# Performance work log

Hardware: AMD Instinct MI355X
Metric: run time of the kernel (lower is better)

## Reference

```python
import jax, jax.numpy as jnp
import numpy as np

HIDDEN = 1024
HEADS = 16
HEAD_DIM = HIDDEN // HEADS


def setup_inputs() -> dict:
    key = jax.random.key(0)
    ks = jax.random.split(key, 9)
    s = 1.0 / np.sqrt(HIDDEN)
    inp = {
        "x": jax.random.normal(ks[0], (4, 2048, HIDDEN), dtype=jnp.float32),
        "wq": jax.random.uniform(ks[1], (HIDDEN, HIDDEN), jnp.float32, -s, s),
        "bq": jax.random.uniform(ks[2], (HIDDEN,), jnp.float32, -s, s),
        "wk": jax.random.uniform(ks[3], (HIDDEN, HIDDEN), jnp.float32, -s, s),
        "bk": jax.random.uniform(ks[4], (HIDDEN,), jnp.float32, -s, s),
        "wv": jax.random.uniform(ks[5], (HIDDEN, HIDDEN), jnp.float32, -s, s),
        "bv": jax.random.uniform(ks[6], (HIDDEN,), jnp.float32, -s, s),
        "wo": jax.random.uniform(ks[7], (HIDDEN, HIDDEN), jnp.float32, -s, s),
        "bo": jax.random.uniform(ks[8], (HIDDEN,), jnp.float32, -s, s),
    }
    return inp


def reference(x, wq, bq, wk, bk, wv, bv, wo, bo):
    B, S, D = x.shape
    H, Hd = HEADS, HEAD_DIM
    # torch Linear: y = x @ W.T + b
    def split_heads(t):  # [B,S,D] -> [B,H,S,Hd]
        return t.reshape(B, S, H, Hd).transpose(0, 2, 1, 3)
    q = split_heads(x @ wq.T + bq)
    k = split_heads(x @ wk.T + bk)
    v = split_heads(x @ wv.T + bv)
    scores = jnp.einsum('bhqd,bhkd->bhqk', q, k) / jnp.sqrt(jnp.float32(Hd))
    attn = jax.nn.softmax(scores, axis=-1)  # dropout is identity in eval
    ctx = jnp.einsum('bhqk,bhkd->bhqd', attn, v)
    ctx = ctx.transpose(0, 2, 1, 3).reshape(B, S, D)
    pooled = ctx.mean(axis=1)  # [B, D]
    out = pooled @ wo.T + bo
    return out, attn.mean(axis=1)
```

## Files before the change

### kernel.cpp

```cpp
#include <hip/hip_runtime.h>

#define B_ 4
#define S_ 2048
#define D_ 1024
#define H_ 16
#define HD_ 64
#define M_ 8192

typedef __attribute__((ext_vector_type(8))) short          bf16x8;
typedef __attribute__((ext_vector_type(8))) unsigned short u16x8;
typedef __attribute__((ext_vector_type(4))) float          f32x4;

#define MFMA16(a, b, c) __builtin_amdgcn_mfma_f32_16x16x32_bf16((a), (b), (c), 0, 0, 0)

#define SCL 0.18033688011112042f

__device__ __forceinline__ unsigned short f2b(float f) {
    unsigned int u = __float_as_uint(f);
    return (unsigned short)((u + 0x7fffu + ((u >> 16) & 1u)) >> 16);
}

__device__ __forceinline__ unsigned int cvtpk_bf16(float lo, float hi) {
    unsigned int r;
    asm("v_cvt_pk_bf16_f32 %0, %1, %2" : "=v"(r) : "v"(lo), "v"(hi));
    return r;
}

__global__ __launch_bounds__(256) void cast_k(const float* __restrict__ src,
                                              unsigned short* __restrict__ dst, int n) {
    int i = (blockIdx.x * 256 + threadIdx.x) * 4;
    if (i >= n) return;
    float4 v = *(const float4*)(src + i);
    ushort4 o;
    o.x = f2b(v.x); o.y = f2b(v.y); o.z = f2b(v.z); o.w = f2b(v.w);
    *(ushort4*)(dst + i) = o;
}

__global__ __launch_bounds__(256) void cast3_k(
    const float* __restrict__ s0, const float* __restrict__ s1, const float* __restrict__ s2,
    unsigned short* __restrict__ d0, unsigned short* __restrict__ d1,
    unsigned short* __restrict__ d2, int n) {
    const float* src = (blockIdx.y == 0) ? s0 : (blockIdx.y == 1) ? s1 : s2;
    unsigned short* dst = (blockIdx.y == 0) ? d0 : (blockIdx.y == 1) ? d1 : d2;
    int i = (blockIdx.x * 256 + threadIdx.x) * 4;
    if (i >= n) return;
    float4 v = *(const float4*)(src + i);
    ushort4 o;
    o.x = f2b(v.x); o.y = f2b(v.y); o.z = f2b(v.z); o.w = f2b(v.w);
    *(ushort4*)(dst + i) = o;
}

__global__ __launch_bounds__(256) void qkv_gemm_k(
    const unsigned short* __restrict__ xb,
    const unsigned short* __restrict__ wb0, const unsigned short* __restrict__ wb1,
    const unsigned short* __restrict__ wb2,
    const float* __restrict__ bq, const float* __restrict__ bk, const float* __restrict__ bv,
    unsigned short* __restrict__ Qo, unsigned short* __restrict__ Ko,
    unsigned short* __restrict__ VT)
{
    __shared__ unsigned short xs[128][72];
    __shared__ unsigned short wsm[128][72];

    const unsigned short* W; const float* bias;
    if (blockIdx.z == 0)      { W = wb0; bias = bq; }
    else if (blockIdx.z == 1) { W = wb1; bias = bk; }
    else                      { W = wb2; bias = bv; }

    const int m0 = blockIdx.x * 128, n0 = blockIdx.y * 128;
    const int tid = threadIdx.x, lane = tid & 63, wid = tid >> 6;
    const int wm = (wid >> 1) * 64, wn = (wid & 1) * 64;
    const int srow = tid >> 3;
    const int skc  = (tid & 7) * 8;

    f32x4 acc[4][4] = {};

    for (int k0 = 0; k0 < D_; k0 += 64) {
        u16x8 xa[4], wa[4];
        #pragma unroll
        for (int r = 0; r < 4; ++r) {
            int row = srow + 32 * r;
            xa[r] = *(const u16x8*)&xb[(size_t)(m0 + row) * D_ + k0 + skc];
            wa[r] = *(const u16x8*)&W [(size_t)(n0 + row) * D_ + k0 + skc];
        }
        __syncthreads();
        #pragma unroll
        for (int r = 0; r < 4; ++r) {
            int row = srow + 32 * r;
            *(u16x8*)&xs[row][skc]  = xa[r];
            *(u16x8*)&wsm[row][skc] = wa[r];
        }
        __syncthreads();
        #pragma unroll
        for (int kd = 0; kd < 2; ++kd) {
            const int kc = 32 * kd + 8 * (lane >> 4);
            bf16x8 af[4], bfr[4];
            #pragma unroll
            for (int mf = 0; mf < 4; ++mf)
                af[mf] = *(const bf16x8*)&xs[wm + 16 * mf + (lane & 15)][kc];
            #pragma unroll
            for (int nf = 0; nf < 4; ++nf)
                bfr[nf] = *(const bf16x8*)&wsm[wn + 16 * nf + (lane & 15)][kc];
            #pragma unroll
            for (int mf = 0; mf < 4; ++mf)
                #pragma unroll
                for (int nf = 0; nf < 4; ++nf)
                    acc[mf][nf] = MFMA16(af[mf], bfr[nf], acc[mf][nf]);
        }
    }

    const int col_l = lane & 15, rgrp = lane >> 4;
    if (blockIdx.z != 2) {
        unsigned short* out = (blockIdx.z == 0) ? Qo : Ko;
        const float oscale = (blockIdx.z == 0) ? SCL : 1.0f;
        #pragma unroll
        for (int nf = 0; nf < 4; ++nf) {
            const int n = n0 + wn + 16 * nf + col_l;
            const float bval = bias[n];
            const int h = n >> 6, d = n & 63;
            #pragma unroll
            for (int mf = 0; mf < 4; ++mf)
                #pragma unroll
                for (int r = 0; r < 4; ++r) {
                    int m = m0 + wm + 16 * mf + 4 * rgrp + r;
                    int bI = m >> 11, s = m & 2047;
                    out[(((size_t)bI * H_ + h) * S_ + s) * HD_ + d]
                        = f2b((acc[mf][nf][r] + bval) * oscale);
                }
        }
    } else {
        #pragma unroll
        for (int nf = 0; nf < 4; ++nf) {
            const int n = n0 + wn + 16 * nf + col_l;
            const float bval = bias[n];
            const int h = n >> 6, d = n & 63;
            #pragma unroll
            for (int mf = 0; mf < 4; ++mf) {
                int m = m0 + wm + 16 * mf + 4 * rgrp;
                int bI = m >> 11, s = m & 2047;
                ushort4 o;
                o.x = f2b(acc[mf][nf][0] + bval);
                o.y = f2b(acc[mf][nf][1] + bval);
                o.z = f2b(acc[mf][nf][2] + bval);
                o.w = f2b(acc[mf][nf][3] + bval);
                *(ushort4*)&VT[(((size_t)bI * H_ + h) * HD_ + d) * S_ + s] = o;
            }
        }
    }
}

__global__ __launch_bounds__(256) void attn_ctx_k(
    const unsigned short* __restrict__ Q, const unsigned short* __restrict__ K,
    const unsigned short* __restrict__ VT,
    float* __restrict__ L, float* __restrict__ PPOOL)
{
    __shared__ unsigned short ks[64][72];
    __shared__ unsigned short vt[64][72];
    __shared__ unsigned short ps[128][72];
    __shared__ float pp[4][64];
    __shared__ float lsm[4][32];

    const int lin = blockIdx.x;
    const int g   = (lin & 7) | ((lin >> 7) << 3);
    const int qb  = (lin >> 3) & 15;
    const int b   = g >> 4, h = g & 15;
    const int q0  = qb * 128;

    const size_t hoff = ((size_t)(b * H_ + h)) * S_ * HD_;
    const unsigned short* Qh  = Q  + hoff;
    const unsigned short* Kh  = K  + hoff;
    const unsigned short* VTh = VT + hoff;

    const int tid = threadIdx.x, lane = tid & 63, wid = tid >> 6;
    const int srow = tid >> 3;
    const int skc  = (tid & 7) * 8;
    const int col_l = lane & 15, rgrp = lane >> 4;

    bf16x8 qf[2][2];
    #pragma unroll
    for (int i = 0; i < 2; ++i)
        #pragma unroll
        for (int kd = 0; kd < 2; ++kd)
            qf[i][kd] = *(const bf16x8*)&Qh[(size_t)(q0 + 32 * wid + 16 * i + col_l) * HD_
                                            + 32 * kd + 8 * rgrp];

    f32x4 cacc[2][4] = {};
    float lp[2] = {};

    for (int kb = 0; kb < S_; kb += 64) {
        u16x8 ka[2], va[2];
        #pragma unroll
        for (int r = 0; r < 2; ++r) {
            int row = srow + 32 * r;
            ka[r] = *(const u16x8*)&Kh [(size_t)(kb + row) * HD_ + skc];
            va[r] = *(const u16x8*)&VTh[(size_t)row * S_ + kb + skc];
        }
        __syncthreads();
        #pragma unroll
        for (int r = 0; r < 2; ++r) {
            int row = srow + 32 * r;
            *(u16x8*)&ks[row][skc] = ka[r];
            *(u16x8*)&vt[row][skc] = va[r];
        }
        __syncthreads();

        #pragma unroll
        for (int n = 0; n < 4; ++n) {
            f32x4 s0 = {}, s1 = {};
            #pragma unroll
            for (int kd = 0; kd < 2; ++kd) {
                const int kc = 32 * kd + 8 * rgrp;
                bf16x8 kf = *(const bf16x8*)&ks[16 * n + col_l][kc];
                s0 = MFMA16(kf, qf[0][kd], s0);
                s1 = MFMA16(kf, qf[1][kd], s1);
            }
            float e0 = exp2f(s0[0]), e1 = exp2f(s0[1]), e2 = exp2f(s0[2]), e3 = exp2f(s0[3]);
            lp[0] += (e0 + e1) + (e2 + e3);
            uint2 w0 = { cvtpk_bf16(e0, e1), cvtpk_bf16(e2, e3) };
            *(uint2*)&ps[32 * wid + col_l][16 * n + 4 * rgrp] = w0;
            float f0 = exp2f(s1[0]), f1 = exp2f(s1[1]), f2 = exp2f(s1[2]), f3 = exp2f(s1[3]);
            lp[1] += (f0 + f1) + (f2 + f3);
            uint2 w1 = { cvtpk_bf16(f0, f1), cvtpk_bf16(f2, f3) };
            *(uint2*)&ps[32 * wid + 16 + col_l][16 * n + 4 * rgrp] = w1;
        }

        #pragma unroll
        for (int kk = 0; kk < 2; ++kk) {
            const int kc = 32 * kk + 8 * rgrp;
            bf16x8 pa[2], vf[4];
            #pragma unroll
            for (int i = 0; i < 2; ++i)
                pa[i] = *(const bf16x8*)&ps[32 * wid + 16 * i + col_l][kc];
            #pragma unroll
            for (int n = 0; n < 4; ++n)
                vf[n] = *(const bf16x8*)&vt[16 * n + col_l][kc];
            #pragma unroll
            for (int i = 0; i < 2; ++i)
                #pragma unroll
                for (int n = 0; n < 4; ++n)
                    cacc[i][n] = MFMA16(pa[i], vf[n], cacc[i][n]);
        }
    }

    #pragma unroll
    for (int i = 0; i < 2; ++i) {
        float v = lp[i];
        v += __shfl_xor(v, 16); v += __shfl_xor(v, 32);
        lp[i] = v;
    }
    if (lane < 16) {
        #pragma unroll
        for (int i = 0; i < 2; ++i) {
            L[((size_t)(b * H_ + h)) * S_ + q0 + 32 * wid + 16 * i + lane] = lp[i];
            lsm[wid][16 * i + lane] = lp[i];
        }
    }

    float pool4[4] = {};
    #pragma unroll
    for (int i = 0; i < 2; ++i)
        #pragma unroll
        for (int r = 0; r < 4; ++r) {
            float inv = 1.0f / lsm[wid][16 * i + 4 * rgrp + r];
            #pragma unroll
            for (int n = 0; n < 4; ++n)
                pool4[n] = fmaf(cacc[i][n][r], inv, pool4[n]);
        }
    #pragma unroll
    for (int n = 0; n < 4; ++n) {
        float v = pool4[n];
        v += __shfl_xor(v, 16); v += __shfl_xor(v, 32);
        pool4[n] = v;
    }
    if (lane < 16) {
        #pragma unroll
        for (int n = 0; n < 4; ++n) pp[wid][16 * n + lane] = pool4[n];
    }
    __syncthreads();
    if (tid < 64) {
        float s = pp[0][tid] + pp[1][tid] + pp[2][tid] + pp[3][tid];
        PPOOL[((size_t)(b * H_ + h) * (S_ / 128) + qb) * 64 + tid] = s;
    }
}

__global__ __launch_bounds__(256) void attn_mean_k(
    const unsigned short* __restrict__ Q, const unsigned short* __restrict__ K,
    const float* __restrict__ L, float* __restrict__ attn_out)
{
    __shared__ unsigned short qs[128][72];
    __shared__ unsigned short ksm[64][72];
    __shared__ float lsm[128];

    const int k0 = blockIdx.x * 64, q0 = blockIdx.y * 128, b = blockIdx.z;
    const int tid = threadIdx.x, lane = tid & 63, wid = tid >> 6;
    const int col_l = lane & 15, rgrp = lane >> 4;
    const int qrow = tid >> 1, qcol = (tid & 1) * 32;
    const int krow = tid >> 2, kcol = (tid & 3) * 16;

    f32x4 macc[4][2] = {};

    for (int h = 0; h < H_; ++h) {
        const size_t hoff = ((size_t)(b * H_ + h)) * S_ * HD_;
        const unsigned short* Qh = Q + hoff;
        const unsigned short* Kh = K + hoff;

        u16x8 qa[4], ka[2];
        #pragma unroll
        for (int j = 0; j < 4; ++j)
            qa[j] = *(const u16x8*)&Qh[(size_t)(q0 + qrow) * HD_ + qcol + 8 * j];
        #pragma unroll
        for (int j = 0; j < 2; ++j)
            ka[j] = *(const u16x8*)&Kh[(size_t)(k0 + krow) * HD_ + kcol + 8 * j];
        float lval = 0.f;
        if (tid < 128) lval = L[((size_t)(b * H_ + h)) * S_ + q0 + tid];

        __syncthreads();
        #pragma unroll
        for (int j = 0; j < 4; ++j) *(u16x8*)&qs[qrow][qcol + 8 * j] = qa[j];
        #pragma unroll
        for (int j = 0; j < 2; ++j) *(u16x8*)&ksm[krow][kcol + 8 * j] = ka[j];
        if (tid < 128) lsm[tid] = lval;
        __syncthreads();

        bf16x8 qf[2][2];
        #pragma unroll
        for (int i = 0; i < 2; ++i)
            #pragma unroll
            for (int kd = 0; kd < 2; ++kd)
                qf[i][kd] = *(const bf16x8*)&qs[32 * wid + 16 * i + col_l][32 * kd + 8 * rgrp];

        float li0 = 0.0625f / lsm[32 * wid + col_l];
        float li1 = 0.0625f / lsm[32 * wid + 16 + col_l];

        #pragma unroll
        for (int n = 0; n < 4; ++n) {
            f32x4 s0 = {}, s1 = {};
            #pragma unroll
            for (int kd = 0; kd < 2; ++kd) {
                bf16x8 kf = *(const bf16x8*)&ksm[16 * n + col_l][32 * kd + 8 * rgrp];
                s0 = MFMA16(kf, qf[0][kd], s0);
                s1 = MFMA16(kf, qf[1][kd], s1);
            }
            #pragma unroll
            for (int r = 0; r < 4; ++r) {
                macc[n][0][r] = fmaf(exp2f(s0[r]), li0, macc[n][0][r]);
                macc[n][1][r] = fmaf(exp2f(s1[r]), li1, macc[n][1][r]);
            }
        }
    }

    #pragma unroll
    for (int n = 0; n < 4; ++n)
        #pragma unroll
        for (int i = 0; i < 2; ++i) {
            int q = q0 + 32 * wid + 16 * i + col_l;
            *(f32x4*)&attn_out[((size_t)b * S_ + q) * S_ + k0 + 16 * n + 4 * rgrp]
                = macc[n][i];
        }
}

__global__ __launch_bounds__(256) void out_k(
    const float* __restrict__ PPOOL, const float* __restrict__ wo,
    const float* __restrict__ bo, float* __restrict__ out)
{
    __shared__ float psm[D_];
    const int b = blockIdx.x >> 2;
    for (int d = threadIdx.x; d < D_; d += 256) {
        const float* pp = PPOOL + ((size_t)(b * H_ + (d >> 6)) * (S_ / 128)) * 64 + (d & 63);
        float s = 0.f;
        #pragma unroll
        for (int qb = 0; qb < S_ / 128; ++qb) s += pp[qb * 64];
        psm[d] = s * (1.0f / S_);
    }
    __syncthreads();
    const int j = (blockIdx.x & 3) * 256 + threadIdx.x;
    float sum = bo[j];
    const float* wr = wo + (size_t)j * D_;
    for (int d = 0; d < D_; d += 4) {
        float4 w4 = *(const float4*)&wr[d];
        sum += psm[d] * w4.x + psm[d+1] * w4.y + psm[d+2] * w4.z + psm[d+3] * w4.w;
    }
    out[b * D_ + j] = sum;
}

extern "C" void kernel_launch(void* const* d_in, const int* in_sizes, int n_in,
                              void* d_out, int out_size, void* d_ws, size_t ws_size,
                              hipStream_t stream)
{
    const float* x  = (const float*)d_in[0];
    const float* wq = (const float*)d_in[1];
    const float* bq = (const float*)d_in[2];
    const float* wk = (const float*)d_in[3];
    const float* bk = (const float*)d_in[4];
    const float* wv = (const float*)d_in[5];
    const float* bv = (const float*)d_in[6];
    const float* wo = (const float*)d_in[7];
    const float* bo = (const float*)d_in[8];
    float* out = (float*)d_out;

    char* ws = (char*)d_ws;
    const size_t XN  = (size_t)M_ * D_;
    const size_t WN  = (size_t)D_ * D_;
    const size_t QN  = (size_t)B_ * H_ * S_ * HD_;

    unsigned short* xb  = (unsigned short*)ws;                 ws += XN * 2;
    unsigned short* wqb = (unsigned short*)ws;                 ws += WN * 2;
    unsigned short* wkb = (unsigned short*)ws;                 ws += WN * 2;
    unsigned short* wvb = (unsigned short*)ws;                 ws += WN * 2;
    unsigned short* Qb  = (unsigned short*)ws;                 ws += QN * 2;
    unsigned short* Kb  = (unsigned short*)ws;                 ws += QN * 2;
    unsigned short* VTb = (unsigned short*)ws;                 ws += QN * 2;
    float* Lb    = (float*)ws;                                 ws += (size_t)B_ * H_ * S_ * 4;
    float* PPOOL = (float*)ws;

    cast_k<<<dim3(XN / 1024), 256, 0, stream>>>(x, xb, (int)XN);
    cast3_k<<<dim3(WN / 1024, 3), 256, 0, stream>>>(wq, wk, wv, wqb, wkb, wvb, (int)WN);

    qkv_gemm_k<<<dim3(M_ / 128, D_ / 128, 3), 256, 0, stream>>>(
        xb, wqb, wkb, wvb, bq, bk, bv, Qb, Kb, VTb);
    attn_ctx_k<<<dim3(1024), 256, 0, stream>>>(Qb, Kb, VTb, Lb, PPOOL);
    attn_mean_k<<<dim3(S_ / 64, S_ / 128, B_), 256, 0, stream>>>(Qb, Kb, Lb, out + B_ * D_);
    out_k<<<16, 256, 0, stream>>>(PPOOL, wo, bo, out);
}
```

Before: 404.1 us.

## Swizzle attention LDS tiles, interleave per-row-block softmax with PV, store inverse row sums

In the attention-context kernel, the padded K, V^T and P shared-memory tiles become dense 64x64 tiles. They use an XOR swizzle on 16-byte chunks, which avoids bank conflicts without padding. The score/exp/PV sequence now runs one 16-row query block at a time, so each wave reuses a 16-row P slice and the P buffer shrinks by half. This lowers LDS footprint and may raise occupancy. The kernel also writes reciprocal row sums instead of raw sums, so the attention-mean kernel multiplies instead of divides in its head loop.

```diff
diff --git a/kernel.cpp b/kernel.cpp
--- a/kernel.cpp
+++ b/kernel.cpp
@@ -24,6 +24,12 @@
     unsigned int r;
     asm("v_cvt_pk_bf16_f32 %0, %1, %2" : "=v"(r) : "v"(lo), "v"(hi));
     return r;
+}
+
+__device__ __forceinline__ unsigned short* swz64(unsigned short* base, int row, int col) {
+    unsigned off = ((unsigned)row << 7) + ((unsigned)col << 1);
+    off ^= (unsigned)((row & 7) << 4);
+    return (unsigned short*)((char*)base + off);
 }
 
 __global__ __launch_bounds__(256) void cast_k(const float* __restrict__ src,
@@ -151,11 +157,11 @@
 __global__ __launch_bounds__(256) void attn_ctx_k(
     const unsigned short* __restrict__ Q, const unsigned short* __restrict__ K,
     const unsigned short* __restrict__ VT,
-    float* __restrict__ L, float* __restrict__ PPOOL)
+    float* __restrict__ Linv, float* __restrict__ PPOOL)
 {
-    __shared__ unsigned short ks[64][72];
-    __shared__ unsigned short vt[64][72];
-    __shared__ unsigned short ps[128][72];
+    __shared__ unsigned short ks0[64 * 64];
+    __shared__ unsigned short vt0[64 * 64];
+    __shared__ unsigned short ps0[64 * 64];
     __shared__ float pp[4][64];
     __shared__ float lsm[4][32];
 
@@ -198,46 +204,42 @@
         #pragma unroll
         for (int r = 0; r < 2; ++r) {
             int row = srow + 32 * r;
-            *(u16x8*)&ks[row][skc] = ka[r];
-            *(u16x8*)&vt[row][skc] = va[r];
-        }
-        __syncthreads();
-
-        #pragma unroll
-        for (int n = 0; n < 4; ++n) {
-            f32x4 s0 = {}, s1 = {};
-            #pragma unroll
-            for (int kd = 0; kd < 2; ++kd) {
-                const int kc = 32 * kd + 8 * rgrp;
-                bf16x8 kf = *(const bf16x8*)&ks[16 * n + col_l][kc];
-                s0 = MFMA16(kf, qf[0][kd], s0);
-                s1 = MFMA16(kf, qf[1][kd], s1);
-            }
-            float e0 = exp2f(s0[0]), e1 = exp2f(s0[1]), e2 = exp2f(s0[2]), e3 = exp2f(s0[3]);
-            lp[0] += (e0 + e1) + (e2 + e3);
-            uint2 w0 = { cvtpk_bf16(e0, e1), cvtpk_bf16(e2, e3) };
-            *(uint2*)&ps[32 * wid + col_l][16 * n + 4 * rgrp] = w0;
-            float f0 = exp2f(s1[0]), f1 = exp2f(s1[1]), f2 = exp2f(s1[2]), f3 = exp2f(s1[3]);
-            lp[1] += (f0 + f1) + (f2 + f3);
-            uint2 w1 = { cvtpk_bf16(f0, f1), cvtpk_bf16(f2, f3) };
-            *(uint2*)&ps[32 * wid + 16 + col_l][16 * n + 4 * rgrp] = w1;
-        }
-
-        #pragma unroll
-        for (int kk = 0; kk < 2; ++kk) {
-            const int kc = 32 * kk + 8 * rgrp;
-            bf16x8 pa[2], vf[4];
-            #pragma unroll
-            for (int i = 0; i < 2; ++i)
-                pa[i] = *(const bf16x8*)&ps[32 * wid + 16 * i + col_l][kc];
-            #pragma unroll
-            for (int n = 0; n < 4; ++n)
-                vf[n] = *(const bf16x8*)&vt[16 * n + col_l][kc];
-            #pragma unroll
-            for (int i = 0; i < 2; ++i)
+            *(u16x8*)swz64(ks0, row, skc) = ka[r];
+            *(u16x8*)swz64(vt0, row, skc) = va[r];
+        }
+        __syncthreads();
+
+        #pragma unroll
+        for (int i = 0; i < 2; ++i) {
+            unsigned int w[8];
+            #pragma unroll
+            for (int n = 0; n < 4; ++n) {
+                f32x4 s = {};
                 #pragma unroll
-                for (int n = 0; n < 4; ++n)
-                    cacc[i][n] = MFMA16(pa[i], vf[n], cacc[i][n]);
+                for (int kd = 0; kd < 2; ++kd) {
+                    bf16x8 kf = *(const bf16x8*)swz64(ks0, 16 * n + col_l, 32 * kd + 8 * rgrp);
+                    s = MFMA16(kf, qf[i][kd], s);
+                }
+                float e0 = exp2f(s[0]), e1 = exp2f(s[1]);
+                float e2 = exp2f(s[2]), e3 = exp2f(s[3]);
+                lp[i] += (e0 + e1) + (e2 + e3);
+                w[2 * n]     = cvtpk_bf16(e0, e1);
+                w[2 * n + 1] = cvtpk_bf16(e2, e3);
+            }
+            #pragma unroll
+            for (int n = 0; n < 4; ++n) {
+                uint2 wpair = { w[2 * n], w[2 * n + 1] };
+                *(uint2*)swz64(ps0, 16 * wid + col_l, 16 * n + 4 * rgrp) = wpair;
+            }
+            #pragma unroll
+            for (int kk = 0; kk < 2; ++kk) {
+                bf16x8 pa = *(const bf16x8*)swz64(ps0, 16 * wid + col_l, 32 * kk + 8 * rgrp);
+                #pragma unroll
+                for (int nd = 0; nd < 4; ++nd) {
+                    bf16x8 vf = *(const bf16x8*)swz64(vt0, 16 * nd + col_l, 32 * kk + 8 * rgrp);
+                    cacc[i][nd] = MFMA16(pa, vf, cacc[i][nd]);
+                }
+            }
         }
     }
 
@@ -250,8 +252,9 @@
     if (lane < 16) {
         #pragma unroll
         for (int i = 0; i < 2; ++i) {
-            L[((size_t)(b * H_ + h)) * S_ + q0 + 32 * wid + 16 * i + lane] = lp[i];
-            lsm[wid][16 * i + lane] = lp[i];
+            float inv = 1.0f / lp[i];
+            Linv[((size_t)(b * H_ + h)) * S_ + q0 + 32 * wid + 16 * i + lane] = inv;
+            lsm[wid][16 * i + lane] = inv;
         }
     }
 
@@ -260,7 +263,7 @@
     for (int i = 0; i < 2; ++i)
         #pragma unroll
         for (int r = 0; r < 4; ++r) {
-            float inv = 1.0f / lsm[wid][16 * i + 4 * rgrp + r];
+            float inv = lsm[wid][16 * i + 4 * rgrp + r];
             #pragma unroll
             for (int n = 0; n < 4; ++n)
                 pool4[n] = fmaf(cacc[i][n][r], inv, pool4[n]);
@@ -284,7 +287,7 @@
 
 __global__ __launch_bounds__(256) void attn_mean_k(
     const unsigned short* __restrict__ Q, const unsigned short* __restrict__ K,
-    const float* __restrict__ L, float* __restrict__ attn_out)
+    const float* __restrict__ Linv, float* __restrict__ attn_out)
 {
     __shared__ unsigned short qs[128][72];
     __shared__ unsigned short ksm[64][72];
@@ -311,7 +314,7 @@
         for (int j = 0; j < 2; ++j)
             ka[j] = *(const u16x8*)&Kh[(size_t)(k0 + krow) * HD_ + kcol + 8 * j];
         float lval = 0.f;
-        if (tid < 128) lval = L[((size_t)(b * H_ + h)) * S_ + q0 + tid];
+        if (tid < 128) lval = Linv[((size_t)(b * H_ + h)) * S_ + q0 + tid];
 
         __syncthreads();
         #pragma unroll
@@ -328,8 +331,8 @@
             for (int kd = 0; kd < 2; ++kd)
                 qf[i][kd] = *(const bf16x8*)&qs[32 * wid + 16 * i + col_l][32 * kd + 8 * rgrp];
 
-        float li0 = 0.0625f / lsm[32 * wid + col_l];
-        float li1 = 0.0625f / lsm[32 * wid + 16 + col_l];
+        float li0 = lsm[32 * wid + col_l] * 0.0625f;
+        float li1 = lsm[32 * wid + 16 + col_l] * 0.0625f;
 
         #pragma unroll
         for (int n = 0; n < 4; ++n) {
```

Measured after the change: 426.7 us. 5.6% more time.
